# Performance work log

Measured on AMD Instinct MI355X. Metric: run time of the kernel, lower is better.

The kernel has to match this reference:

```python
import jax, jax.numpy as jnp
import numpy as np

B, S, E, H = 4, 4096, 512, 64


def setup_inputs() -> dict:
    key = jax.random.key(0)
    ks = jax.random.split(key, 6)
    query = jax.random.normal(ks[0], (B, S, E), dtype=jnp.float32)
    key_t = jax.random.normal(ks[1], (B, S, E), dtype=jnp.float32)
    value = jax.random.normal(ks[2], (B, S, E), dtype=jnp.float32)
    # nn.Linear weights are [out, in] = [H, E]; biases [H]
    Wq = jax.random.normal(ks[3], (H, E), dtype=jnp.float32) * 0.02
    Wk = jax.random.normal(ks[4], (H, E), dtype=jnp.float32) * 0.02
    Wv = jax.random.normal(ks[5], (H, E), dtype=jnp.float32) * 0.02
    bq = jnp.zeros((H,), jnp.float32)
    bk = jnp.zeros((H,), jnp.float32)
    bv = jnp.zeros((H,), jnp.float32)
    # causal mask, broadcast over batch; masked_fill where mask == 0
    mask = jnp.tril(jnp.ones((1, S, S), dtype=jnp.bool_))
    return {"query": query, "key": key_t, "value": value,
            "Wq": Wq, "bq": bq, "Wk": Wk, "bk": bk, "Wv": Wv, "bv": bv,
            "mask": mask}


def reference(query, key, value, Wq, bq, Wk, bk, Wv, bv, mask):
    # Bug-faithful: d_k is the LAST dim of the *input* query, i.e. embed_dim
    d_k = query.shape[-1]
    q = jnp.einsum('bse,he->bsh', query, Wq) + bq   # [B,S,H]
    k = jnp.einsum('bse,he->bsh', key, Wk) + bk     # [B,S,H]
    v = jnp.einsum('bse,he->bsh', value, Wv) + bv   # [B,S,H]
    scores = jnp.einsum('bqh,bkh->bqk', q, k) / jnp.sqrt(jnp.float32(d_k))  # [B,S,S]
    scores = jnp.where(mask, scores, -jnp.inf)
    weights = jax.nn.softmax(scores, axis=-1)
    # dropout_rate = 0.0 -> Dropout is identity
    out = jnp.einsum('bqk,bkh->bqh', weights, v)    # [B,S,H]
    return out
```

## Files before the change

kernel.cpp:

```cpp
#include <hip/hip_runtime.h>
#include <hip/hip_bf16.h>
#include <math.h>

typedef unsigned short u16;
typedef unsigned int   u32;
typedef __attribute__((ext_vector_type(8)))  short bf16x8_t;
typedef __attribute__((ext_vector_type(4)))  float f32x4_t;
typedef __attribute__((ext_vector_type(16))) float f32x16_t;
typedef __attribute__((ext_vector_type(4)))  int   i32x4_t;
typedef __attribute__((ext_vector_type(2)))  u32   u32x2_t;

#define SEQ 4096
#define EMB 512
#define HD  64
#define NBATCH 4
#define C2 0.063758718f

#define NPAIR 136
#define SLOTS (NBATCH * NPAIR * 8)

__device__ __forceinline__ u16 to_bf(float f) {
    __hip_bfloat16 h = __float2bfloat16(f);
    return __builtin_bit_cast(u16, h);
}

__device__ __forceinline__ void stage16(const u16* g, u16* l) {
    __builtin_amdgcn_global_load_lds(
        (const __attribute__((address_space(1))) void*)g,
        (__attribute__((address_space(3))) void*)l, 16, 0, 0);
}

__global__ __launch_bounds__(256)
void proj_kernel(const float* __restrict__ q_in, const float* __restrict__ k_in,
                 const float* __restrict__ v_in,
                 const float* __restrict__ Wq, const float* __restrict__ bq,
                 const float* __restrict__ Wk, const float* __restrict__ bk,
                 const float* __restrict__ Wv, const float* __restrict__ bv,
                 u16* __restrict__ outQ, u16* __restrict__ outK,
                 u16* __restrict__ outVT)
{
    const int z = blockIdx.y;
    const float* in   = (z == 0) ? q_in : (z == 1) ? k_in : v_in;
    const float* W    = (z == 0) ? Wq   : (z == 1) ? Wk   : Wv;
    const float* bias = (z == 0) ? bq   : (z == 1) ? bk   : bv;

    __shared__ u16 W_lds[64][264];

    const int tid  = threadIdx.x;
    const int lane = tid & 63;
    const int w    = tid >> 6;
    const int l15  = lane & 15;
    const int lg   = lane >> 4;
    const int g0   = blockIdx.x * 64;

    const float* arow = in + (size_t)(g0 + w * 16 + l15) * EMB + 8 * lg;

    f32x4_t acc[4];
    #pragma unroll
    for (int i = 0; i < 4; ++i)
        #pragma unroll
        for (int j = 0; j < 4; ++j) acc[i][j] = 0.f;

    const int sr = tid >> 2;
    const int sc = (tid & 3) * 64;

    #pragma unroll 1
    for (int half = 0; half < 2; ++half) {
        if (half) __syncthreads();
        {
            const float* src = W + (size_t)sr * EMB + half * 256 + sc;
            #pragma unroll
            for (int u = 0; u < 8; ++u) {
                f32x4_t f0 = *reinterpret_cast<const f32x4_t*>(src + 8 * u);
                f32x4_t f1 = *reinterpret_cast<const f32x4_t*>(src + 8 * u + 4);
                u16 tmp[8];
                #pragma unroll
                for (int e = 0; e < 4; ++e) { tmp[e] = to_bf(f0[e]); tmp[4 + e] = to_bf(f1[e]); }
                *reinterpret_cast<i32x4_t*>(&W_lds[sr][sc + 8 * u]) =
                    *reinterpret_cast<const i32x4_t*>(tmp);
            }
        }
        __syncthreads();

        const float* abase = arow + half * 256;
        #pragma unroll 4
        for (int kt = 0; kt < 8; ++kt) {
            f32x4_t a0 = *reinterpret_cast<const f32x4_t*>(abase + kt * 32);
            f32x4_t a1 = *reinterpret_cast<const f32x4_t*>(abase + kt * 32 + 4);
            u16 ta[8];
            #pragma unroll
            for (int e = 0; e < 4; ++e) { ta[e] = to_bf(a0[e]); ta[4 + e] = to_bf(a1[e]); }
            bf16x8_t af = *reinterpret_cast<const bf16x8_t*>(ta);
            #pragma unroll
            for (int kn = 0; kn < 4; ++kn) {
                bf16x8_t bfrag = *reinterpret_cast<const bf16x8_t*>(
                    &W_lds[kn * 16 + l15][kt * 32 + 8 * lg]);
                acc[kn] = __builtin_amdgcn_mfma_f32_16x16x32_bf16(af, bfrag, acc[kn], 0, 0, 0);
            }
        }
    }

    #pragma unroll
    for (int kn = 0; kn < 4; ++kn) {
        const int col = kn * 16 + l15;
        const float bb = bias[col];
        #pragma unroll
        for (int j = 0; j < 4; ++j) {
            const int grow = g0 + w * 16 + lg * 4 + j;
            const u16 val = to_bf(acc[kn][j] + bb);
            if (z == 0) {
                outQ[(size_t)grow * HD + col] = val;
            } else if (z == 1) {
                outK[(size_t)grow * HD + col] = val;
            } else {
                const int b = grow >> 12, s = grow & (SEQ - 1);
                outVT[((size_t)(b * HD + col)) * SEQ + s] = val;
            }
        }
    }
}

__global__ __launch_bounds__(512, 4)
void attn8_kernel(const u16* __restrict__ Q, const u16* __restrict__ K,
                  const u16* __restrict__ VT,
                  u16* __restrict__ partO, float* __restrict__ partL)
{
    __shared__ u16 Kt[2][64 * 64];
    __shared__ u16 Vt[2][64 * 64];
    __shared__ u16 Pt[8][32 * 64];

    const int tid  = threadIdx.x;
    const int w    = tid >> 6;
    const int lane = tid & 63;
    const int q31  = lane & 31;
    const int half = lane >> 5;

    const int b = blockIdx.y;
    const int y = blockIdx.x;
    int g = 0;
    while ((g + 1) * (g + 2) / 2 <= y) ++g;
    const int c = y - g * (g + 1) / 2;

    const int R0   = 256 * g + 32 * w;
    const int q_g  = R0 + q31;
    const int nt_w = 4 * g + (w >> 1) + 1;
    const int t0   = 4 * c, t1 = 4 * c + 4;

    const u16* Kb  = K  + (size_t)b * SEQ * HD;
    const u16* VTb = VT + (size_t)b * HD * SEQ;

    const int srow = w * 8 + (lane >> 3);
    const int schk = (lane & 7) ^ ((lane >> 3) & 7);

    bf16x8_t qf0, qf1, qf2, qf3;
    {
        const u16* qp = Q + ((size_t)b * SEQ + q_g) * HD + 8 * half;
        qf0 = *(const bf16x8_t*)(qp + 0);
        qf1 = *(const bf16x8_t*)(qp + 16);
        qf2 = *(const bf16x8_t*)(qp + 32);
        qf3 = *(const bf16x8_t*)(qp + 48);
    }

    f32x16_t acc0, acc1;
    #pragma unroll
    for (int i = 0; i < 16; ++i) { acc0[i] = 0.f; acc1[i] = 0.f; }
    float lsum = 0.f;

    auto STAGE = [&](int u, int t) {
        stage16(&Kb[((size_t)(t * 64 + srow)) * HD + schk * 8], &Kt[u][w * 512]);
        stage16(&VTb[(size_t)srow * SEQ + t * 64 + schk * 8],   &Vt[u][w * 512]);
    };

    STAGE(0, t0);
    asm volatile("s_waitcnt vmcnt(0)" ::: "memory");
    __syncthreads();

    for (int t = t0; t < t1; ++t) {
        const int u = (t - t0) & 1;
        if (t + 1 < t1) STAGE(u ^ 1, t + 1);
        if (t < nt_w) {
            const bool last = (t == nt_w - 1);
            #pragma unroll
            for (int ksub = 0; ksub < 2; ++ksub) {
                f32x16_t sf;
                #pragma unroll
                for (int i = 0; i < 16; ++i) sf[i] = 0.f;
                const int kl = ksub * 32 + q31;
                #pragma unroll
                for (int s = 0; s < 4; ++s) {
                    bf16x8_t a = *(const bf16x8_t*)
                        &Kt[u][kl * 64 + ((s * 16 + 8 * half) ^ ((kl & 7) << 3))];
                    bf16x8_t qq = (s == 0) ? qf0 : (s == 1) ? qf1 : (s == 2) ? qf2 : qf3;
                    sf = __builtin_amdgcn_mfma_f32_32x32x16_bf16(a, qq, sf, 0, 0, 0);
                }
                #pragma unroll
                for (int j = 0; j < 4; ++j) {
                    float p[4];
                    #pragma unroll
                    for (int e = 0; e < 4; ++e) {
                        const int kk    = 8 * j + 4 * half + e;
                        const int key_g = t * 64 + ksub * 32 + kk;
                        float v = exp2f(sf[4 * j + e] * C2);
                        if (last && key_g > q_g) v = 0.f;
                        lsum += v;
                        p[e] = v;
                    }
                    u32x2_t pk;
                    pk[0] = (u32)to_bf(p[0]) | ((u32)to_bf(p[1]) << 16);
                    pk[1] = (u32)to_bf(p[2]) | ((u32)to_bf(p[3]) << 16);
                    const int col = (ksub * 32 + 8 * j + 4 * half) ^ ((q31 & 7) << 3);
                    *(u32x2_t*)&Pt[w][q31 * 64 + col] = pk;
                }
            }
            asm volatile("s_waitcnt lgkmcnt(0)" ::: "memory");
            __builtin_amdgcn_sched_barrier(0);
            #pragma unroll
            for (int kp = 0; kp < 4; ++kp) {
                bf16x8_t pb = *(const bf16x8_t*)
                    &Pt[w][q31 * 64 + ((kp * 16 + 8 * half) ^ ((q31 & 7) << 3))];
                {
                    const int dl = q31;
                    bf16x8_t va = *(const bf16x8_t*)
                        &Vt[u][dl * 64 + ((kp * 16 + 8 * half) ^ ((dl & 7) << 3))];
                    acc0 = __builtin_amdgcn_mfma_f32_32x32x16_bf16(va, pb, acc0, 0, 0, 0);
                }
                {
                    const int dl = 32 + q31;
                    bf16x8_t va = *(const bf16x8_t*)
                        &Vt[u][dl * 64 + ((kp * 16 + 8 * half) ^ ((dl & 7) << 3))];
                    acc1 = __builtin_amdgcn_mfma_f32_32x32x16_bf16(va, pb, acc1, 0, 0, 0);
                }
            }
        }
        asm volatile("s_waitcnt vmcnt(0)" ::: "memory");
        __syncthreads();
    }

    lsum += __shfl_xor(lsum, 32);
    const int slot = (b * NPAIR + y) * 8 + w;
    u16* po = partO + (size_t)slot * 2048;
    #pragma unroll
    for (int dsub = 0; dsub < 2; ++dsub) {
        #pragma unroll
        for (int j = 0; j < 4; ++j) {
            const f32x16_t& a = dsub ? acc1 : acc0;
            u32x2_t pk;
            pk[0] = (u32)to_bf(a[4 * j + 0]) | ((u32)to_bf(a[4 * j + 1]) << 16);
            pk[1] = (u32)to_bf(a[4 * j + 2]) | ((u32)to_bf(a[4 * j + 3]) << 16);
            const int d = 32 * dsub + 8 * j + 4 * half;
            *(u32x2_t*)&po[q31 * 64 + d] = pk;
        }
    }
    if (half == 0) partL[(size_t)slot * 32 + q31] = lsum;
}

__global__ __launch_bounds__(256)
void reduce8_kernel(const u16* __restrict__ partO, const float* __restrict__ partL,
                    float* __restrict__ out)
{
    const int x  = blockIdx.x;
    const int b  = x >> 7;
    const int gw = x & 127;
    const int g  = gw >> 3;
    const int w  = gw & 7;
    const int ybase = g * (g + 1) / 2;

    const int t  = threadIdx.x;
    const int q  = t >> 3;
    const int d0 = (t & 7) * 8;

    float acc[8];
    #pragma unroll
    for (int i = 0; i < 8; ++i) acc[i] = 0.f;
    float l = 0.f;

    for (int c = 0; c <= g; ++c) {
        const int slot = (b * NPAIR + ybase + c) * 8 + w;
        i32x4_t raw = *(const i32x4_t*)(partO + (size_t)slot * 2048 + q * 64 + d0);
        const u16* pr = (const u16*)&raw;
        #pragma unroll
        for (int i = 0; i < 8; ++i) {
            u32 bits = ((u32)pr[i]) << 16;
            acc[i] += __builtin_bit_cast(float, bits);
        }
        l += partL[(size_t)slot * 32 + q];
    }
    const float inv = 1.f / l;
    f32x4_t r0, r1;
    #pragma unroll
    for (int i = 0; i < 4; ++i) { r0[i] = acc[i] * inv; r1[i] = acc[4 + i] * inv; }
    const size_t row = (size_t)b * SEQ + g * 256 + w * 32 + q;
    *(f32x4_t*)&out[row * HD + d0]     = r0;
    *(f32x4_t*)&out[row * HD + d0 + 4] = r1;
}

extern "C" void kernel_launch(void* const* d_in, const int* in_sizes, int n_in,
                              void* d_out, int out_size, void* d_ws, size_t ws_size,
                              hipStream_t stream)
{
    const float* q_in = (const float*)d_in[0];
    const float* k_in = (const float*)d_in[1];
    const float* v_in = (const float*)d_in[2];
    const float* Wq   = (const float*)d_in[3];
    const float* bq   = (const float*)d_in[4];
    const float* Wk   = (const float*)d_in[5];
    const float* bk   = (const float*)d_in[6];
    const float* Wv   = (const float*)d_in[7];
    const float* bv   = (const float*)d_in[8];
    float* out = (float*)d_out;

    const size_t NQ = (size_t)NBATCH * SEQ * HD;
    u16* wsQ   = (u16*)d_ws;
    u16* wsK   = wsQ + NQ;
    u16* wsVT  = wsK + NQ;
    u16* partO = wsVT + NQ;
    float* partL = (float*)(partO + (size_t)SLOTS * 2048);

    proj_kernel<<<dim3(256, 3), 256, 0, stream>>>(q_in, k_in, v_in, Wq, bq, Wk, bk,
                                                  Wv, bv, wsQ, wsK, wsVT);
    attn8_kernel<<<dim3(NPAIR, NBATCH), 512, 0, stream>>>(wsQ, wsK, wsVT, partO, partL);
    reduce8_kernel<<<dim3(512), 256, 0, stream>>>(partO, partL, out);
}
```

Measured before the change: 73.85 us.

## Pipeline activation loads through triple-buffered swizzled LDS in projection kernel

The projection kernel now converts the whole weight matrix to bf16 in LDS once, instead of in two halves. Activation tiles are streamed into a three-deep LDS ring with direct global-to-LDS loads, using an XOR swizzle and explicit vmcnt waits so loads overlap the MFMA work. Bias values are also prefetched into registers at kernel start. The cost is much more LDS per block (about 115KB), which may lower occupancy, plus hand-tuned wait counts that depend on the instruction order.

After: 78.90 us. 1.07x slower.

```diff
diff --git a/kernel.cpp b/kernel.cpp
--- a/kernel.cpp
+++ b/kernel.cpp
@@ -24,7 +24,7 @@
     return __builtin_bit_cast(u16, h);
 }
 
-__device__ __forceinline__ void stage16(const u16* g, u16* l) {
+__device__ __forceinline__ void stage16(const void* g, void* l) {
     __builtin_amdgcn_global_load_lds(
         (const __attribute__((address_space(1))) void*)g,
         (__attribute__((address_space(3))) void*)l, 16, 0, 0);
@@ -44,7 +44,8 @@
     const float* W    = (z == 0) ? Wq   : (z == 1) ? Wk   : Wv;
     const float* bias = (z == 0) ? bq   : (z == 1) ? bk   : bv;
 
-    __shared__ u16 W_lds[64][264];
+    __shared__ __align__(16) u16   W_lds[64][520];
+    __shared__ __align__(16) float A_lds[3][64][64];
 
     const int tid  = threadIdx.x;
     const int lane = tid & 63;
@@ -53,7 +54,37 @@
     const int lg   = lane >> 4;
     const int g0   = blockIdx.x * 64;
 
-    const float* arow = in + (size_t)(g0 + w * 16 + l15) * EMB + 8 * lg;
+    float bvals[4];
+    #pragma unroll
+    for (int kn = 0; kn < 4; ++kn) bvals[kn] = bias[kn * 16 + l15];
+    asm volatile("" :: "v"(bvals[0]), "v"(bvals[1]), "v"(bvals[2]), "v"(bvals[3]));
+
+    {
+        const int row = tid >> 2;
+        const int cb  = (tid & 3) * 128;
+        const float* src = W + (size_t)row * EMB + cb;
+        #pragma unroll
+        for (int u = 0; u < 16; ++u) {
+            f32x4_t f0 = *reinterpret_cast<const f32x4_t*>(src + 8 * u);
+            f32x4_t f1 = *reinterpret_cast<const f32x4_t*>(src + 8 * u + 4);
+            u16 tmp[8];
+            #pragma unroll
+            for (int e = 0; e < 4; ++e) { tmp[e] = to_bf(f0[e]); tmp[4 + e] = to_bf(f1[e]); }
+            *reinterpret_cast<i32x4_t*>(&W_lds[row][cb + 8 * u]) =
+                *reinterpret_cast<const i32x4_t*>(tmp);
+        }
+    }
+    __syncthreads();
+
+    auto STAGE_A = [&](int buf, int t) {
+        #pragma unroll
+        for (int i = 0; i < 4; ++i) {
+            const int rl = w * 16 + i * 4 + (lane >> 4);
+            const int cs = (lane & 15) ^ (rl & 7);
+            stage16(in + (size_t)(g0 + rl) * EMB + t * 64 + cs * 4,
+                    &A_lds[buf][w * 16 + i * 4][0]);
+        }
+    };
 
     f32x4_t acc[4];
     #pragma unroll
@@ -61,32 +92,27 @@
         #pragma unroll
         for (int j = 0; j < 4; ++j) acc[i][j] = 0.f;
 
-    const int sr = tid >> 2;
-    const int sc = (tid & 3) * 64;
-
-    #pragma unroll 1
-    for (int half = 0; half < 2; ++half) {
-        if (half) __syncthreads();
-        {
-            const float* src = W + (size_t)sr * EMB + half * 256 + sc;
-            #pragma unroll
-            for (int u = 0; u < 8; ++u) {
-                f32x4_t f0 = *reinterpret_cast<const f32x4_t*>(src + 8 * u);
-                f32x4_t f1 = *reinterpret_cast<const f32x4_t*>(src + 8 * u + 4);
-                u16 tmp[8];
-                #pragma unroll
-                for (int e = 0; e < 4; ++e) { tmp[e] = to_bf(f0[e]); tmp[4 + e] = to_bf(f1[e]); }
-                *reinterpret_cast<i32x4_t*>(&W_lds[sr][sc + 8 * u]) =
-                    *reinterpret_cast<const i32x4_t*>(tmp);
-            }
-        }
-        __syncthreads();
-
-        const float* abase = arow + half * 256;
-        #pragma unroll 4
-        for (int kt = 0; kt < 8; ++kt) {
-            f32x4_t a0 = *reinterpret_cast<const f32x4_t*>(abase + kt * 32);
-            f32x4_t a1 = *reinterpret_cast<const f32x4_t*>(abase + kt * 32 + 4);
+    const int rswz = l15 & 7;
+
+    STAGE_A(0, 0);
+    STAGE_A(1, 1);
+
+    #pragma unroll
+    for (int kt = 0; kt < 8; ++kt) {
+        const int buf = kt % 3;
+        if (kt < 6) STAGE_A((kt + 2) % 3, kt + 2);
+        if (kt < 6)      asm volatile("s_waitcnt vmcnt(8)" ::: "memory");
+        else if (kt == 6) asm volatile("s_waitcnt vmcnt(4)" ::: "memory");
+        else              asm volatile("s_waitcnt vmcnt(0)" ::: "memory");
+        __builtin_amdgcn_sched_barrier(0);
+
+        #pragma unroll
+        for (int ks = 0; ks < 2; ++ks) {
+            const int c0 = ks * 8 + lg * 2;
+            f32x4_t a0 = *reinterpret_cast<const f32x4_t*>(
+                &A_lds[buf][w * 16 + l15][((c0)     ^ rswz) * 4]);
+            f32x4_t a1 = *reinterpret_cast<const f32x4_t*>(
+                &A_lds[buf][w * 16 + l15][((c0 + 1) ^ rswz) * 4]);
             u16 ta[8];
             #pragma unroll
             for (int e = 0; e < 4; ++e) { ta[e] = to_bf(a0[e]); ta[4 + e] = to_bf(a1[e]); }
@@ -94,7 +120,7 @@
             #pragma unroll
             for (int kn = 0; kn < 4; ++kn) {
                 bf16x8_t bfrag = *reinterpret_cast<const bf16x8_t*>(
-                    &W_lds[kn * 16 + l15][kt * 32 + 8 * lg]);
+                    &W_lds[kn * 16 + l15][kt * 64 + ks * 32 + 8 * lg]);
                 acc[kn] = __builtin_amdgcn_mfma_f32_16x16x32_bf16(af, bfrag, acc[kn], 0, 0, 0);
             }
         }
@@ -103,11 +129,10 @@
     #pragma unroll
     for (int kn = 0; kn < 4; ++kn) {
         const int col = kn * 16 + l15;
-        const float bb = bias[col];
         #pragma unroll
         for (int j = 0; j < 4; ++j) {
             const int grow = g0 + w * 16 + lg * 4 + j;
-            const u16 val = to_bf(acc[kn][j] + bb);
+            const u16 val = to_bf(acc[kn][j] + bvals[kn]);
             if (z == 0) {
                 outQ[(size_t)grow * HD + col] = val;
             } else if (z == 1) {
```

## Pre-convert weights to bf16 fragment layout and pipeline projection loads

Applied to the files above, without the earlier changes.

Adds a small kernel that converts the three weight matrices to bf16 once, stored in MFMA fragment order in workspace. The projection kernel then reads the weight fragments straight from global memory instead of having every block convert W into LDS behind barriers. It also software-pipelines the input and weight loads four k-steps ahead. The cost is an extra kernel launch and more registers for the in-flight buffers. The weight buffer reuses the partO workspace, which the attention kernel later overwrites.

After: 72.05 us. -2.4%, faster.

```diff
diff --git a/kernel.cpp b/kernel.cpp
--- a/kernel.cpp
+++ b/kernel.cpp
@@ -24,27 +24,47 @@
     return __builtin_bit_cast(u16, h);
 }
 
-__device__ __forceinline__ void stage16(const u16* g, u16* l) {
+__device__ __forceinline__ void stage16(const void* g, void* l) {
     __builtin_amdgcn_global_load_lds(
         (const __attribute__((address_space(1))) void*)g,
         (__attribute__((address_space(3))) void*)l, 16, 0, 0);
 }
 
 __global__ __launch_bounds__(256)
+void wprep_kernel(const float* __restrict__ Wq, const float* __restrict__ Wk,
+                  const float* __restrict__ Wv, u16* __restrict__ wbf)
+{
+    const int zkt = blockIdx.x;
+    const int z   = zkt >> 4;
+    const int kt  = zkt & 15;
+    const float* W = (z == 0) ? Wq : (z == 1) ? Wk : Wv;
+    const int kn   = threadIdx.x >> 6;
+    const int lane = threadIdx.x & 63;
+    const int l15  = lane & 15;
+    const int lg   = lane >> 4;
+
+    const float* src = W + (size_t)(kn * 16 + l15) * EMB + kt * 32 + lg * 8;
+    f32x4_t f0 = *reinterpret_cast<const f32x4_t*>(src);
+    f32x4_t f1 = *reinterpret_cast<const f32x4_t*>(src + 4);
+    u16 tmp[8];
+    #pragma unroll
+    for (int e = 0; e < 4; ++e) { tmp[e] = to_bf(f0[e]); tmp[4 + e] = to_bf(f1[e]); }
+    *reinterpret_cast<i32x4_t*>(
+        &wbf[((size_t)((z * 16 + kt) * 4 + kn)) * 512 + lane * 8]) =
+        *reinterpret_cast<const i32x4_t*>(tmp);
+}
+
+__global__ __launch_bounds__(256, 3)
 void proj_kernel(const float* __restrict__ q_in, const float* __restrict__ k_in,
-                 const float* __restrict__ v_in,
-                 const float* __restrict__ Wq, const float* __restrict__ bq,
-                 const float* __restrict__ Wk, const float* __restrict__ bk,
-                 const float* __restrict__ Wv, const float* __restrict__ bv,
+                 const float* __restrict__ v_in, const u16* __restrict__ wbf,
+                 const float* __restrict__ bq, const float* __restrict__ bk,
+                 const float* __restrict__ bv,
                  u16* __restrict__ outQ, u16* __restrict__ outK,
                  u16* __restrict__ outVT)
 {
     const int z = blockIdx.y;
     const float* in   = (z == 0) ? q_in : (z == 1) ? k_in : v_in;
-    const float* W    = (z == 0) ? Wq   : (z == 1) ? Wk   : Wv;
     const float* bias = (z == 0) ? bq   : (z == 1) ? bk   : bv;
-
-    __shared__ u16 W_lds[64][264];
 
     const int tid  = threadIdx.x;
     const int lane = tid & 63;
@@ -52,8 +72,15 @@
     const int l15  = lane & 15;
     const int lg   = lane >> 4;
     const int g0   = blockIdx.x * 64;
-
-    const float* arow = in + (size_t)(g0 + w * 16 + l15) * EMB + 8 * lg;
+    const int row  = g0 + w * 16 + l15;
+
+    const float* arow = in + (size_t)row * EMB + lg * 8;
+    const u16*   wz   = wbf + (size_t)z * 16 * 4 * 512 + lane * 8;
+
+    float bvals[4];
+    #pragma unroll
+    for (int kn = 0; kn < 4; ++kn) bvals[kn] = bias[kn * 16 + l15];
+    asm volatile("" :: "v"(bvals[0]), "v"(bvals[1]), "v"(bvals[2]), "v"(bvals[3]));
 
     f32x4_t acc[4];
     #pragma unroll
@@ -61,60 +88,50 @@
         #pragma unroll
         for (int j = 0; j < 4; ++j) acc[i][j] = 0.f;
 
-    const int sr = tid >> 2;
-    const int sc = (tid & 3) * 64;
-
-    #pragma unroll 1
-    for (int half = 0; half < 2; ++half) {
-        if (half) __syncthreads();
-        {
-            const float* src = W + (size_t)sr * EMB + half * 256 + sc;
-            #pragma unroll
-            for (int u = 0; u < 8; ++u) {
-                f32x4_t f0 = *reinterpret_cast<const f32x4_t*>(src + 8 * u);
-                f32x4_t f1 = *reinterpret_cast<const f32x4_t*>(src + 8 * u + 4);
-                u16 tmp[8];
-                #pragma unroll
-                for (int e = 0; e < 4; ++e) { tmp[e] = to_bf(f0[e]); tmp[4 + e] = to_bf(f1[e]); }
-                *reinterpret_cast<i32x4_t*>(&W_lds[sr][sc + 8 * u]) =
-                    *reinterpret_cast<const i32x4_t*>(tmp);
-            }
-        }
-        __syncthreads();
-
-        const float* abase = arow + half * 256;
-        #pragma unroll 4
-        for (int kt = 0; kt < 8; ++kt) {
-            f32x4_t a0 = *reinterpret_cast<const f32x4_t*>(abase + kt * 32);
-            f32x4_t a1 = *reinterpret_cast<const f32x4_t*>(abase + kt * 32 + 4);
-            u16 ta[8];
-            #pragma unroll
-            for (int e = 0; e < 4; ++e) { ta[e] = to_bf(a0[e]); ta[4 + e] = to_bf(a1[e]); }
-            bf16x8_t af = *reinterpret_cast<const bf16x8_t*>(ta);
-            #pragma unroll
-            for (int kn = 0; kn < 4; ++kn) {
-                bf16x8_t bfrag = *reinterpret_cast<const bf16x8_t*>(
-                    &W_lds[kn * 16 + l15][kt * 32 + 8 * lg]);
-                acc[kn] = __builtin_amdgcn_mfma_f32_16x16x32_bf16(af, bfrag, acc[kn], 0, 0, 0);
-            }
-        }
-    }
+    f32x4_t  a0[4], a1[4];
+    bf16x8_t wf[4][4];
+
+#define ISSUE(kt)                                                              \
+    {                                                                          \
+        a0[(kt) & 3] = *reinterpret_cast<const f32x4_t*>(arow + (kt) * 32);    \
+        a1[(kt) & 3] = *reinterpret_cast<const f32x4_t*>(arow + (kt) * 32 + 4);\
+        _Pragma("unroll")                                                      \
+        for (int kn = 0; kn < 4; ++kn)                                         \
+            wf[(kt) & 3][kn] = *reinterpret_cast<const bf16x8_t*>(             \
+                wz + ((size_t)((kt) * 4 + kn) << 9));                          \
+    }
+
+    #pragma unroll
+    for (int kt = 0; kt < 4; ++kt) ISSUE(kt);
+
+    #pragma unroll
+    for (int kt = 0; kt < 16; ++kt) {
+        const int s = kt & 3;
+        u16 ta[8];
+        #pragma unroll
+        for (int e = 0; e < 4; ++e) { ta[e] = to_bf(a0[s][e]); ta[4 + e] = to_bf(a1[s][e]); }
+        bf16x8_t af = *reinterpret_cast<const bf16x8_t*>(ta);
+        #pragma unroll
+        for (int kn = 0; kn < 4; ++kn)
+            acc[kn] = __builtin_amdgcn_mfma_f32_16x16x32_bf16(af, wf[s][kn], acc[kn], 0, 0, 0);
+        if (kt < 12) ISSUE(kt + 4);
+    }
+#undef ISSUE
 
     #pragma unroll
     for (int kn = 0; kn < 4; ++kn) {
         const int col = kn * 16 + l15;
-        const float bb = bias[col];
         #pragma unroll
         for (int j = 0; j < 4; ++j) {
             const int grow = g0 + w * 16 + lg * 4 + j;
-            const u16 val = to_bf(acc[kn][j] + bb);
+            const u16 val = to_bf(acc[kn][j] + bvals[kn]);
             if (z == 0) {
                 outQ[(size_t)grow * HD + col] = val;
             } else if (z == 1) {
                 outK[(size_t)grow * HD + col] = val;
             } else {
-                const int b = grow >> 12, s = grow & (SEQ - 1);
-                outVT[((size_t)(b * HD + col)) * SEQ + s] = val;
+                const int b = grow >> 12, s2 = grow & (SEQ - 1);
+                outVT[((size_t)(b * HD + col)) * SEQ + s2] = val;
             }
         }
     }
@@ -315,9 +332,11 @@
     u16* wsVT  = wsK + NQ;
     u16* partO = wsVT + NQ;
     float* partL = (float*)(partO + (size_t)SLOTS * 2048);
-
-    proj_kernel<<<dim3(256, 3), 256, 0, stream>>>(q_in, k_in, v_in, Wq, bq, Wk, bk,
-                                                  Wv, bv, wsQ, wsK, wsVT);
+    u16* wbf = partO;
+
+    wprep_kernel<<<dim3(48), 256, 0, stream>>>(Wq, Wk, Wv, wbf);
+    proj_kernel<<<dim3(256, 3), 256, 0, stream>>>(q_in, k_in, v_in, wbf,
+                                                  bq, bk, bv, wsQ, wsK, wsVT);
     attn8_kernel<<<dim3(NPAIR, NBATCH), 512, 0, stream>>>(wsQ, wsK, wsVT, partO, partL);
     reduce8_kernel<<<dim3(512), 256, 0, stream>>>(partO, partL, out);
 }
```
